# Performance work log

Hardware: AMD Instinct MI355X
Metric: run time of the kernel (lower is better)

The kernel has to match this reference:

```python
import jax, jax.numpy as jnp
import numpy as np

BZ, IN_DIM, STATE_DIM, OUT_DIM, L = 16, 512, 512, 512, 2048
INIT_SCALE = 0.5


def setup_inputs() -> dict:
    key = jax.random.key(0)
    k_u, k_a, k_b, k_c = jax.random.split(key, 4)
    u = jax.random.normal(k_u, (BZ, IN_DIM, L), dtype=jnp.float32)
    A_unconstrained = jax.random.normal(k_a, (STATE_DIM,), dtype=jnp.float32) * 0.1
    B = jax.random.normal(k_b, (STATE_DIM, IN_DIM), dtype=jnp.float32) * INIT_SCALE / np.sqrt(IN_DIM)
    C = jax.random.normal(k_c, (OUT_DIM, STATE_DIM), dtype=jnp.float32) * INIT_SCALE / np.sqrt(STATE_DIM)
    D = jnp.zeros((OUT_DIM, IN_DIM), dtype=jnp.float32)
    h0 = jnp.zeros((STATE_DIM,), dtype=jnp.float32)
    return {"u": u, "A_unconstrained": A_unconstrained, "B": B, "C": C, "D": D, "h0": h0}


def reference(u, A_unconstrained, B, C, D, h0):
    # u: (Bz, input_dim, L)
    Bz = u.shape[0]
    A_diag = -jax.nn.softplus(A_unconstrained)  # (S,)
    # Time-invariant input projection, batched over all timesteps: (L, Bz, S)
    Bu = jnp.einsum('bil,si->lbs', u, B)

    state0 = jnp.broadcast_to(h0[None, :], (Bz, h0.shape[0]))

    def step(state, bu_t):
        x_t = state * A_diag[None, :] + bu_t  # (Bz, S)
        return x_t, x_t

    _, xs = jax.lax.scan(step, state0, Bu)  # xs: (L, Bz, S)

    # Output projection: y_t = C x_t + D u_t  -> (Bz, out, L)
    Y = jnp.einsum('lbs,os->bol', xs, C) + jnp.einsum('bil,oi->bol', u, D)
    return Y
```

## Files before the change

### kernel.cpp

```cpp
#include <hip/hip_runtime.h>
#include <math.h>

typedef __bf16 bf16;
typedef __bf16 bf16x2 __attribute__((ext_vector_type(2)));
typedef __bf16 bf16x4 __attribute__((ext_vector_type(4)));
typedef __bf16 bf16x8 __attribute__((ext_vector_type(8)));
typedef float  f32x4  __attribute__((ext_vector_type(4)));

#define BZd 16
#define INd 512
#define Sd  512
#define Od  512
#define Ld  2048
#define CLd 128
#define NCd (Ld / CLd)

__global__ __launch_bounds__(256) void prep_all(const float* __restrict__ B,
                                                const float* __restrict__ C,
                                                const float* __restrict__ D,
                                                const float* __restrict__ Au,
                                                bf16* __restrict__ Bb, bf16* __restrict__ Cb,
                                                bf16* __restrict__ Db, float* __restrict__ A_diag,
                                                int* __restrict__ dfa) {
    __shared__ int sred[4];
    int bid = blockIdx.x;
    if (bid == 768) {
        #pragma unroll
        for (int r = 0; r < 2; ++r) {
            int ss = threadIdx.x + r * 256;
            float x = Au[ss];
            float sp = fmaxf(x, 0.0f) + log1pf(expf(-fabsf(x)));
            A_diag[ss] = -sp;
        }
        return;
    }
    int which = bid >> 8, lb = bid & 255;
    const float* src = which == 0 ? B : (which == 1 ? C : D);
    bf16* dst = which == 0 ? Bb : (which == 1 ? Cb : Db);
    int i = lb * 256 + threadIdx.x;
    float4 v = *(const float4*)&src[(size_t)i * 4];
    bf16x4 o = { (bf16)v.x, (bf16)v.y, (bf16)v.z, (bf16)v.w };
    *(bf16x4*)&dst[(size_t)i * 4] = o;
    if (which == 2) {
        int nz = (v.x != 0.f) | (v.y != 0.f) | (v.z != 0.f) | (v.w != 0.f);
        unsigned long long bl = __ballot(nz);
        int wv = threadIdx.x >> 6;
        if ((threadIdx.x & 63) == 0) sred[wv] = (bl != 0ull);
        __syncthreads();
        if (threadIdx.x == 0) dfa[lb] = sred[0] | sred[1] | sred[2] | sred[3];
    }
}

__global__ __launch_bounds__(256) void transp_u(const float* __restrict__ u,
                                                bf16* __restrict__ ut) {
    __shared__ bf16 t[64][73];
    int b = blockIdx.z, i0 = blockIdx.y * 64, l0 = blockIdx.x * 64;
    int tid = threadIdx.x, tx = tid & 15, ty = tid >> 4;
    const float* ub = u + ((size_t)b * INd + i0) * Ld + l0;
    #pragma unroll
    for (int r = 0; r < 4; ++r) {
        int il = r * 16 + ty;
        float4 v = *(const float4*)&ub[(size_t)il * Ld + tx * 4];
        t[il][tx * 4 + 0] = (bf16)v.x;
        t[il][tx * 4 + 1] = (bf16)v.y;
        t[il][tx * 4 + 2] = (bf16)v.z;
        t[il][tx * 4 + 3] = (bf16)v.w;
    }
    __syncthreads();
    bf16* uo = ut + ((size_t)b * Ld + l0) * INd + i0;
    #pragma unroll
    for (int it = 0; it < 2; ++it) {
        int q = it * 256 + tid;
        int lr = q >> 3;
        int ic = (q & 7) * 8;
        bf16x8 o;
        #pragma unroll
        for (int e = 0; e < 8; ++e) o[e] = t[ic + e][lr];
        *(bf16x8*)&uo[(size_t)lr * INd + ic] = o;
    }
}

template<bool OBF16>
__global__ __launch_bounds__(512, 2) void gemm8p(
    const bf16* __restrict__ A0, size_t aBS0,
    const bf16* __restrict__ B0, size_t bBS0,
    const bf16* __restrict__ A1, size_t aBS1,
    const bf16* __restrict__ B1, size_t bBS1,
    const int* __restrict__ dfa,
    const float* __restrict__ A_diag, float* __restrict__ cePtr,
    void* __restrict__ OutV, size_t oBS, int ldOut,
    int NX, int NY)
{
    __shared__ bf16 lds[4 * 16384];
    const int tid = threadIdx.x;
    const int lane = tid & 63, w = tid >> 6;

    int nwg = gridDim.x, bid = blockIdx.x;
    int cpx = nwg >> 3;
    int swz = (bid & 7) * cpx + (bid >> 3);
    int pb = NX * NY;
    int b  = swz / pb;
    int r0 = swz - b * pb;
    int by = r0 / NX;
    int bx = r0 - by * NX;

    const int wm = w >> 2, wn = w & 3;
    const int fr = lane & 15, g = lane >> 4;

    int extra = 0;
    if (dfa) {
        int4 f = ((const int4*)dfa)[lane];
        extra = __any((f.x | f.y | f.z | f.w) != 0) ? 1 : 0;
    }
    const int NT = extra ? 16 : 8;
    const int NU = 2 * NT;

    const bf16* Ab0 = A0 + (size_t)b * aBS0 + (size_t)(by * 256) * 512;
    const bf16* Bb0 = B0 + (size_t)b * bBS0 + (size_t)(bx * 256) * 512;
    const bf16* Ab1 = A1 + (size_t)b * aBS1 + (size_t)(by * 256) * 512;
    const bf16* Bb1 = B1 + (size_t)b * bBS1 + (size_t)(bx * 256) * 512;

    f32x4 acc[8][4];
    #pragma unroll
    for (int i = 0; i < 8; ++i)
        #pragma unroll
        for (int j = 0; j < 4; ++j)
            acc[i][j] = (f32x4){0.f, 0.f, 0.f, 0.f};

    auto stage_part = [&](int U, int isB) {
        int T = U >> 1, kh = U & 1;
        const bf16* Mb = isB ? (T >= 8 ? Bb1 : Bb0) : (T >= 8 ? Ab1 : Ab0);
        int kbase = ((T & 7) << 6) + (kh << 5);
        int slot = U & 3;
        #pragma unroll
        for (int rblk = 0; rblk < 2; ++rblk) {
            int row = rblk * 128 + (tid >> 2);
            int pos = tid & 3;
            int cs = pos ^ ((row & 3) ^ ((row >> 2) & 3));
            __builtin_amdgcn_global_load_lds(
                (const __attribute__((address_space(1))) void*)(Mb + (size_t)row * 512 + kbase + cs * 8),
                (__attribute__((address_space(3))) void*)&lds[slot * 16384 + isB * 8192 + (rblk * 128 + w * 16) * 32],
                16, 0, 0);
        }
    };

    stage_part(0, 0); stage_part(0, 1);
    stage_part(1, 0); stage_part(1, 1);
    stage_part(2, 0); stage_part(2, 1);

    bf16x8 av[4], bv[4];
    for (int U = 0; U < NU; ++U) {
        int ahead = NU - 1 - U;
        if (ahead >= 2)      { asm volatile("s_waitcnt vmcnt(8)" ::: "memory"); }
        else if (ahead == 1) { asm volatile("s_waitcnt vmcnt(4)" ::: "memory"); }
        else                 { asm volatile("s_waitcnt vmcnt(0)" ::: "memory"); }
        __builtin_amdgcn_sched_barrier(0);
        __builtin_amdgcn_s_barrier();
        __builtin_amdgcn_sched_barrier(0);

        const bf16* Ls = &lds[(U & 3) * 16384];
        #pragma unroll
        for (int mf = 0; mf < 2; ++mf) {
            if (mf == 1) {
                __builtin_amdgcn_sched_barrier(0);
                __builtin_amdgcn_s_barrier();
                __builtin_amdgcn_sched_barrier(0);
            }
            if (mf == 0) {
                #pragma unroll
                for (int j = 0; j < 4; ++j) {
                    int R = wn * 64 + j * 16 + fr;
                    int pos = g ^ ((R & 3) ^ ((R >> 2) & 3));
                    bv[j] = *(const bf16x8*)&Ls[8192 + R * 32 + pos * 8];
                }
            }
            #pragma unroll
            for (int i = 0; i < 4; ++i) {
                int R = wm * 128 + (mf * 4 + i) * 16 + fr;
                int pos = g ^ ((R & 3) ^ ((R >> 2) & 3));
                av[i] = *(const bf16x8*)&Ls[R * 32 + pos * 8];
            }
            if (U + 3 < NU) stage_part(U + 3, mf);
            asm volatile("s_waitcnt lgkmcnt(0)" ::: "memory");
            __builtin_amdgcn_sched_barrier(0);
            __builtin_amdgcn_s_setprio(1);
            #pragma unroll
            for (int i = 0; i < 4; ++i)
                #pragma unroll
                for (int j = 0; j < 4; ++j)
                    acc[mf * 4 + i][j] = __builtin_amdgcn_mfma_f32_16x16x32_bf16(
                        av[i], bv[j], acc[mf * 4 + i][j], 0, 0, 0);
            __builtin_amdgcn_s_setprio(0);
        }
    }

    if (OBF16 && cePtr) {
        int colBase = bx * 256 + wn * 64;
        #pragma unroll
        for (int j = 0; j < 4; ++j) {
            float a = A_diag[colBase + j * 16 + fr];
            float a2 = a * a, a4 = a2 * a2, a8 = a4 * a4, a16 = a8 * a8;
            float S = 0.f;
            #pragma unroll
            for (int I = 0; I < 8; ++I) {
                f32x4 v = acc[I][j];
                float e = fmaf(fmaf(fmaf(v[0], a, v[1]), a, v[2]), a, v[3]);
                float e0 = __shfl(e, fr);
                float e1 = __shfl(e, fr + 16);
                float e2 = __shfl(e, fr + 32);
                float e3 = __shfl(e, fr + 48);
                float E = fmaf(fmaf(fmaf(e0, a4, e1), a4, e2), a4, e3);
                S = fmaf(S, a16, E);
            }
            if (g == 0)
                cePtr[((size_t)b * NCd + (by * 2 + wm)) * Sd + colBase + j * 16 + fr] = S;
        }
    }

    int m0 = by * 256 + wm * 128 + g * 4;
    int n0 = bx * 256 + wn * 64 + fr;
    if (OBF16) {
        bf16* out = (bf16*)OutV + (size_t)b * oBS;
        #pragma unroll
        for (int i = 0; i < 8; ++i)
            #pragma unroll
            for (int j = 0; j < 4; ++j)
                #pragma unroll
                for (int q = 0; q < 4; ++q)
                    out[(size_t)(m0 + i * 16 + q) * ldOut + n0 + j * 16] = (bf16)acc[i][j][q];
    } else {
        float* out = (float*)OutV + (size_t)b * oBS;
        #pragma unroll
        for (int i = 0; i < 8; ++i)
            #pragma unroll
            for (int j = 0; j < 4; ++j)
                #pragma unroll
                for (int q = 0; q < 4; ++q)
                    out[(size_t)(m0 + i * 16 + q) * ldOut + n0 + j * 16] = acc[i][j][q];
    }
}

__global__ __launch_bounds__(256) void pass_scan2(bf16* __restrict__ xbuf,
                                                  const float* __restrict__ A_diag,
                                                  const float* __restrict__ ce,
                                                  const float* __restrict__ h0) {
    int gI = blockIdx.x * 256 + threadIdx.x;
    int sp = gI & 255;
    int c = (gI >> 8) & (NCd - 1);
    int b = gI >> 12;
    int s = sp * 2;
    float a0 = A_diag[s], a1 = A_diag[s + 1];
    float acl0 = a0, acl1 = a1;
    #pragma unroll
    for (int i = 0; i < 7; ++i) { acl0 *= acl0; acl1 *= acl1; }
    float x0 = h0[s], x1 = h0[s + 1];
    for (int cp = 0; cp < NCd; ++cp) {
        if (cp >= c) break;
        float2 e = *(const float2*)&ce[((size_t)b * NCd + cp) * Sd + s];
        x0 = fmaf(acl0, x0, e.x);
        x1 = fmaf(acl1, x1, e.y);
    }
    bf16* p = xbuf + ((size_t)b * Ld + (size_t)c * CLd) * Sd + s;
    #pragma unroll 4
    for (int j = 0; j < CLd; ++j) {
        bf16x2 v = *(const bf16x2*)&p[(size_t)j * Sd];
        x0 = fmaf(a0, x0, (float)v[0]);
        x1 = fmaf(a1, x1, (float)v[1]);
        bf16x2 o = { (bf16)x0, (bf16)x1 };
        *(bf16x2*)&p[(size_t)j * Sd] = o;
    }
}

extern "C" void kernel_launch(void* const* d_in, const int* in_sizes, int n_in,
                              void* d_out, int out_size, void* d_ws, size_t ws_size,
                              hipStream_t stream) {
    const float* u  = (const float*)d_in[0];
    const float* Au = (const float*)d_in[1];
    const float* Bm = (const float*)d_in[2];
    const float* Cm = (const float*)d_in[3];
    const float* Dm = (const float*)d_in[4];
    const float* h0 = (const float*)d_in[5];
    float* Y = (float*)d_out;

    char* ws = (char*)d_ws;
    bf16* bu = (bf16*)ws;
    bf16* ut = (bf16*)(ws + (32ull << 20));
    bf16* Bb = (bf16*)(ws + (64ull << 20));
    bf16* Cb = Bb + 262144;
    bf16* Db = Cb + 262144;
    float* A_diag = (float*)(ws + (64ull << 20) + 3ull * 524288);
    float* ce   = A_diag + 512;
    int*   dfa  = (int*)(ce + (size_t)BZd * NCd * Sd);

    prep_all<<<769, 256, 0, stream>>>(Bm, Cm, Dm, Au, Bb, Cb, Db, A_diag, dfa);
    transp_u<<<dim3(Ld / 64, INd / 64, BZd), 256, 0, stream>>>(u, ut);

    gemm8p<true><<<(Sd / 256) * (Ld / 256) * BZd, 512, 0, stream>>>(
        ut, (size_t)Ld * INd, Bb, 0,
        ut, (size_t)Ld * INd, Bb, 0,
        nullptr,
        A_diag, ce,
        (void*)bu, (size_t)Ld * Sd, Sd,
        Sd / 256, Ld / 256);

    pass_scan2<<<(BZd * NCd * (Sd / 2)) / 256, 256, 0, stream>>>(bu, A_diag, ce, h0);

    gemm8p<false><<<(Ld / 256) * (Od / 256) * BZd, 512, 0, stream>>>(
        Cb, 0, bu, (size_t)Ld * Sd,
        Db, 0, ut, (size_t)Ld * INd,
        dfa,
        A_diag, nullptr,
        (void*)Y, (size_t)Od * Ld, Ld,
        Ld / 256, Od / 256);
}
```

Before: 97.25 us.

## Fuse u transpose into GEMM and chunk scan into GEMM epilogue with decoupled lookback

Removes the separate transpose kernel by loading fp32 u directly in the first GEMM, transposing and converting it through registers into LDS. Removes the separate scan kernel by doing the intra-tile scan in the GEMM epilogue and chaining carries between tiles via global flags with spin-waits. The D-term is also handled in a separate fallback loop that reads u directly. This cuts two launches and a full read/write pass over the bf16 state buffer, but relies on co-residency of the tiles for the flag spin and adds serialization along the L dimension.

```diff
diff --git a/kernel.cpp b/kernel.cpp
--- a/kernel.cpp
+++ b/kernel.cpp
@@ -2,7 +2,6 @@
 #include <math.h>
 
 typedef __bf16 bf16;
-typedef __bf16 bf16x2 __attribute__((ext_vector_type(2)));
 typedef __bf16 bf16x4 __attribute__((ext_vector_type(4)));
 typedef __bf16 bf16x8 __attribute__((ext_vector_type(8)));
 typedef float  f32x4  __attribute__((ext_vector_type(4)));
@@ -12,8 +11,8 @@
 #define Sd  512
 #define Od  512
 #define Ld  2048
-#define CLd 128
-#define NCd (Ld / CLd)
+
+__device__ __forceinline__ int keyf(int r) { return (r & 3) ^ ((r >> 2) & 3); }
 
 __global__ __launch_bounds__(256) void prep_all(const float* __restrict__ B,
                                                 const float* __restrict__ C,
@@ -21,7 +20,7 @@
                                                 const float* __restrict__ Au,
                                                 bf16* __restrict__ Bb, bf16* __restrict__ Cb,
                                                 bf16* __restrict__ Db, float* __restrict__ A_diag,
-                                                int* __restrict__ dfa) {
+                                                int* __restrict__ dfa, int* __restrict__ flags) {
     __shared__ int sred[4];
     int bid = blockIdx.x;
     if (bid == 768) {
@@ -32,17 +31,18 @@
             float sp = fmaxf(x, 0.0f) + log1pf(expf(-fabsf(x)));
             A_diag[ss] = -sp;
         }
+        flags[threadIdx.x] = 0;
         return;
     }
     int which = bid >> 8, lb = bid & 255;
     const float* src = which == 0 ? B : (which == 1 ? C : D);
     bf16* dst = which == 0 ? Bb : (which == 1 ? Cb : Db);
     int i = lb * 256 + threadIdx.x;
-    float4 v = *(const float4*)&src[(size_t)i * 4];
-    bf16x4 o = { (bf16)v.x, (bf16)v.y, (bf16)v.z, (bf16)v.w };
+    f32x4 v = *(const f32x4*)&src[(size_t)i * 4];
+    bf16x4 o = { (bf16)v[0], (bf16)v[1], (bf16)v[2], (bf16)v[3] };
     *(bf16x4*)&dst[(size_t)i * 4] = o;
     if (which == 2) {
-        int nz = (v.x != 0.f) | (v.y != 0.f) | (v.z != 0.f) | (v.w != 0.f);
+        int nz = (v[0] != 0.f) | (v[1] != 0.f) | (v[2] != 0.f) | (v[3] != 0.f);
         unsigned long long bl = __ballot(nz);
         int wv = threadIdx.x >> 6;
         if ((threadIdx.x & 63) == 0) sred[wv] = (bl != 0ull);
@@ -51,47 +51,24 @@
     }
 }
 
-__global__ __launch_bounds__(256) void transp_u(const float* __restrict__ u,
-                                                bf16* __restrict__ ut) {
-    __shared__ bf16 t[64][73];
-    int b = blockIdx.z, i0 = blockIdx.y * 64, l0 = blockIdx.x * 64;
-    int tid = threadIdx.x, tx = tid & 15, ty = tid >> 4;
-    const float* ub = u + ((size_t)b * INd + i0) * Ld + l0;
-    #pragma unroll
-    for (int r = 0; r < 4; ++r) {
-        int il = r * 16 + ty;
-        float4 v = *(const float4*)&ub[(size_t)il * Ld + tx * 4];
-        t[il][tx * 4 + 0] = (bf16)v.x;
-        t[il][tx * 4 + 1] = (bf16)v.y;
-        t[il][tx * 4 + 2] = (bf16)v.z;
-        t[il][tx * 4 + 3] = (bf16)v.w;
-    }
-    __syncthreads();
-    bf16* uo = ut + ((size_t)b * Ld + l0) * INd + i0;
-    #pragma unroll
-    for (int it = 0; it < 2; ++it) {
-        int q = it * 256 + tid;
-        int lr = q >> 3;
-        int ic = (q & 7) * 8;
-        bf16x8 o;
-        #pragma unroll
-        for (int e = 0; e < 8; ++e) o[e] = t[ic + e][lr];
-        *(bf16x8*)&uo[(size_t)lr * INd + ic] = o;
-    }
-}
-
-template<bool OBF16>
+template<int AREG, int SCAN>
 __global__ __launch_bounds__(512, 2) void gemm8p(
-    const bf16* __restrict__ A0, size_t aBS0,
-    const bf16* __restrict__ B0, size_t bBS0,
-    const bf16* __restrict__ A1, size_t aBS1,
-    const bf16* __restrict__ B1, size_t bBS1,
+    const bf16* __restrict__ Abf, size_t aBS,
+    const float* __restrict__ Uf, size_t uBS,
+    const bf16* __restrict__ Bbf, size_t bBS,
+    const bf16* __restrict__ Dbf,
     const int* __restrict__ dfa,
-    const float* __restrict__ A_diag, float* __restrict__ cePtr,
+    const float* __restrict__ A_diag,
+    const float* __restrict__ h0,
+    float* __restrict__ Lg, int* __restrict__ flags,
     void* __restrict__ OutV, size_t oBS, int ldOut,
     int NX, int NY)
 {
-    __shared__ bf16 lds[4 * 16384];
+    constexpr int RS   = AREG ? 40 : 32;
+    constexpr int ASZ  = 256 * RS;
+    constexpr int SLOT = ASZ + 256 * 32;
+    __shared__ bf16 lds[4 * SLOT];
+
     const int tid = threadIdx.x;
     const int lane = tid & 63, w = tid >> 6;
 
@@ -106,19 +83,17 @@
 
     const int wm = w >> 2, wn = w & 3;
     const int fr = lane & 15, g = lane >> 4;
+    const int iq = tid & 7, lq = tid >> 3;
+
+    const bf16*  Ab = AREG ? nullptr : (Abf + (size_t)b * aBS + (size_t)(by * 256) * 512);
+    const float* Ub = Uf ? (Uf + (size_t)b * uBS) : nullptr;
+    const bf16*  Bp = Bbf + (size_t)b * bBS + (size_t)(bx * 256) * 512;
 
     int extra = 0;
-    if (dfa) {
+    if (!AREG && dfa) {
         int4 f = ((const int4*)dfa)[lane];
         extra = __any((f.x | f.y | f.z | f.w) != 0) ? 1 : 0;
     }
-    const int NT = extra ? 16 : 8;
-    const int NU = 2 * NT;
-
-    const bf16* Ab0 = A0 + (size_t)b * aBS0 + (size_t)(by * 256) * 512;
-    const bf16* Bb0 = B0 + (size_t)b * bBS0 + (size_t)(bx * 256) * 512;
-    const bf16* Ab1 = A1 + (size_t)b * aBS1 + (size_t)(by * 256) * 512;
-    const bf16* Bb1 = B1 + (size_t)b * bBS1 + (size_t)(bx * 256) * 512;
 
     f32x4 acc[8][4];
     #pragma unroll
@@ -127,99 +102,225 @@
         for (int j = 0; j < 4; ++j)
             acc[i][j] = (f32x4){0.f, 0.f, 0.f, 0.f};
 
-    auto stage_part = [&](int U, int isB) {
-        int T = U >> 1, kh = U & 1;
-        const bf16* Mb = isB ? (T >= 8 ? Bb1 : Bb0) : (T >= 8 ? Ab1 : Ab0);
-        int kbase = ((T & 7) << 6) + (kh << 5);
-        int slot = U & 3;
-        #pragma unroll
-        for (int rblk = 0; rblk < 2; ++rblk) {
-            int row = rblk * 128 + (tid >> 2);
-            int pos = tid & 3;
-            int cs = pos ^ ((row & 3) ^ ((row >> 2) & 3));
-            __builtin_amdgcn_global_load_lds(
-                (const __attribute__((address_space(1))) void*)(Mb + (size_t)row * 512 + kbase + cs * 8),
-                (__attribute__((address_space(3))) void*)&lds[slot * 16384 + isB * 8192 + (rblk * 128 + w * 16) * 32],
-                16, 0, 0);
-        }
-    };
-
-    stage_part(0, 0); stage_part(0, 1);
-    stage_part(1, 0); stage_part(1, 1);
-    stage_part(2, 0); stage_part(2, 1);
-
-    bf16x8 av[4], bv[4];
-    for (int U = 0; U < NU; ++U) {
-        int ahead = NU - 1 - U;
-        if (ahead >= 2)      { asm volatile("s_waitcnt vmcnt(8)" ::: "memory"); }
-        else if (ahead == 1) { asm volatile("s_waitcnt vmcnt(4)" ::: "memory"); }
-        else                 { asm volatile("s_waitcnt vmcnt(0)" ::: "memory"); }
+    f32x4 areg[4];
+
+    #define GLD16(srcP, dstElem) __builtin_amdgcn_global_load_lds( \
+        (const __attribute__((address_space(1))) void*)(srcP), \
+        (__attribute__((address_space(3))) void*)&lds[dstElem], 16, 0, 0)
+
+    auto gldA = [&](int U) {
+        #pragma unroll
+        for (int rb = 0; rb < 2; ++rb) {
+            int row = rb * 128 + (tid >> 2);
+            int cs = (tid & 3) ^ keyf(row);
+            GLD16(Ab + (size_t)row * 512 + U * 32 + cs * 8,
+                  (U & 3) * SLOT + (rb * 128 + w * 16) * 32);
+        }
+    };
+    auto gldB = [&](int U) {
+        #pragma unroll
+        for (int rb = 0; rb < 2; ++rb) {
+            int row = rb * 128 + (tid >> 2);
+            int cs = (tid & 3) ^ keyf(row);
+            GLD16(Bp + (size_t)row * 512 + U * 32 + cs * 8,
+                  (U & 3) * SLOT + ASZ + (rb * 128 + w * 16) * 32);
+        }
+    };
+    auto issueA = [&](int U) {
+        #pragma unroll
+        for (int d = 0; d < 4; ++d)
+            areg[d] = *(const f32x4*)&Ub[(size_t)(U * 32 + iq * 4 + d) * Ld + by * 256 + lq * 4];
+    };
+    auto writeA = [&](int U) {
+        bf16* As = &lds[(U & 3) * SLOT];
+        #pragma unroll
+        for (int dl = 0; dl < 4; ++dl) {
+            int r = lq * 4 + dl;
+            bf16x4 wv = { (bf16)areg[0][dl], (bf16)areg[1][dl], (bf16)areg[2][dl], (bf16)areg[3][dl] };
+            *(bf16x4*)&As[r * RS + iq * 4] = wv;
+        }
+    };
+    auto readFrags = [&](int slot, bf16x8* avf, bf16x8* bvf) {
+        const bf16* As = &lds[slot * SLOT];
+        const bf16* Bs = &lds[slot * SLOT + ASZ];
+        #pragma unroll
+        for (int i = 0; i < 8; ++i) {
+            int R = wm * 128 + i * 16 + fr;
+            if (AREG) avf[i] = *(const bf16x8*)&As[R * RS + g * 8];
+            else      avf[i] = *(const bf16x8*)&As[R * RS + (g ^ keyf(R)) * 8];
+        }
+        #pragma unroll
+        for (int j = 0; j < 4; ++j) {
+            int R = wn * 64 + j * 16 + fr;
+            bvf[j] = *(const bf16x8*)&Bs[R * 32 + (g ^ keyf(R)) * 8];
+        }
+    };
+
+    if (AREG) { issueA(0); gldB(0); gldB(1); }
+    else      { gldA(0); gldB(0); gldA(1); gldB(1); }
+
+    for (int U = 0; U < 16; ++U) {
+        if (U < 15) {
+            if (AREG) asm volatile("s_waitcnt vmcnt(2)" ::: "memory");
+            else      asm volatile("s_waitcnt vmcnt(4)" ::: "memory");
+        } else {
+            asm volatile("s_waitcnt vmcnt(0)" ::: "memory");
+        }
         __builtin_amdgcn_sched_barrier(0);
+        if (AREG) {
+            writeA(U);
+            asm volatile("s_waitcnt lgkmcnt(0)" ::: "memory");
+        }
         __builtin_amdgcn_s_barrier();
         __builtin_amdgcn_sched_barrier(0);
-
-        const bf16* Ls = &lds[(U & 3) * 16384];
-        #pragma unroll
-        for (int mf = 0; mf < 2; ++mf) {
-            if (mf == 1) {
-                __builtin_amdgcn_sched_barrier(0);
+        bf16x8 av[8], bv[4];
+        readFrags(U & 3, av, bv);
+        if (AREG) { if (U + 1 < 16) issueA(U + 1); }
+        else      { if (U + 2 < 16) gldA(U + 2); }
+        if (U + 2 < 16) gldB(U + 2);
+        __builtin_amdgcn_s_setprio(1);
+        #pragma unroll
+        for (int i = 0; i < 8; ++i)
+            #pragma unroll
+            for (int j = 0; j < 4; ++j)
+                acc[i][j] = __builtin_amdgcn_mfma_f32_16x16x32_bf16(av[i], bv[j], acc[i][j], 0, 0, 0);
+        __builtin_amdgcn_s_setprio(0);
+    }
+
+    if (!AREG) {
+        if (extra) {
+            #pragma unroll 1
+            for (int T = 0; T < 16; ++T) {
+                int k0 = T * 32;
                 __builtin_amdgcn_s_barrier();
-                __builtin_amdgcn_sched_barrier(0);
+                f32x4 r4[4];
+                #pragma unroll
+                for (int d = 0; d < 4; ++d)
+                    r4[d] = *(const f32x4*)&Ub[(size_t)(k0 + iq * 4 + d) * Ld + bx * 256 + lq * 4];
+                #pragma unroll
+                for (int rb = 0; rb < 2; ++rb) {
+                    int row = rb * 128 + (tid >> 2);
+                    int cs = (tid & 3) ^ keyf(row);
+                    GLD16(Dbf + (size_t)(by * 256 + row) * 512 + k0 + cs * 8,
+                          (rb * 128 + w * 16) * 32);
+                }
+                asm volatile("s_waitcnt vmcnt(0)" ::: "memory");
+                #pragma unroll
+                for (int dl = 0; dl < 4; ++dl) {
+                    int r = lq * 4 + dl;
+                    bf16x4 wv = { (bf16)r4[0][dl], (bf16)r4[1][dl], (bf16)r4[2][dl], (bf16)r4[3][dl] };
+                    int e = ((iq >> 1) ^ keyf(r)) * 8 + (iq & 1) * 4;
+                    *(bf16x4*)&lds[ASZ + r * 32 + e] = wv;
+                }
+                asm volatile("s_waitcnt lgkmcnt(0)" ::: "memory");
+                __builtin_amdgcn_s_barrier();
+                bf16x8 av[8], bv[4];
+                readFrags(0, av, bv);
+                #pragma unroll
+                for (int i = 0; i < 8; ++i)
+                    #pragma unroll
+                    for (int j = 0; j < 4; ++j)
+                        acc[i][j] = __builtin_amdgcn_mfma_f32_16x16x32_bf16(av[i], bv[j], acc[i][j], 0, 0, 0);
             }
-            if (mf == 0) {
-                #pragma unroll
-                for (int j = 0; j < 4; ++j) {
-                    int R = wn * 64 + j * 16 + fr;
-                    int pos = g ^ ((R & 3) ^ ((R >> 2) & 3));
-                    bv[j] = *(const bf16x8*)&Ls[8192 + R * 32 + pos * 8];
-                }
+        }
+    }
+
+    int n0 = bx * 256 + wn * 64 + fr;
+    int m0 = by * 256 + wm * 128 + g * 4;
+
+    if (SCAN) {
+        float av_[4], a2_[4], a4_[4], a16_[4], a128_[4], a256_[4], A4G_[4];
+        #pragma unroll
+        for (int j = 0; j < 4; ++j) {
+            float a = A_diag[n0 + j * 16];
+            float a2 = a * a, a4 = a2 * a2, a8 = a4 * a4, a16 = a8 * a8;
+            float a32 = a16 * a16, a64 = a32 * a32, a128 = a64 * a64;
+            av_[j] = a; a2_[j] = a2; a4_[j] = a4; a16_[j] = a16;
+            a128_[j] = a128; a256_[j] = a128 * a128;
+            A4G_[j] = (g == 0) ? 1.0f : (g == 1) ? a4 : (g == 2) ? a8 : a8 * a4;
+        }
+        float P8[4];
+        #pragma unroll
+        for (int j = 0; j < 4; ++j) {
+            float a = av_[j], a4 = a4_[j], a16 = a16_[j];
+            float P = 0.0f;
+            #pragma unroll
+            for (int i = 0; i < 8; ++i) {
+                f32x4 v = acc[i][j];
+                float e = fmaf(fmaf(fmaf(v[0], a, v[1]), a, v[2]), a, v[3]);
+                float e0 = __shfl(e, fr), e1 = __shfl(e, fr + 16);
+                float e2 = __shfl(e, fr + 32), e3 = __shfl(e, fr + 48);
+                float E = fmaf(fmaf(fmaf(e0, a4, e1), a4, e2), a4, e3);
+                float h2 = fmaf(e0, a4, e1), h3 = fmaf(h2, a4, e2);
+                float PG = (g == 0) ? 0.0f : (g == 1) ? e0 : (g == 2) ? h2 : h3;
+                float Vg = fmaf(A4G_[j], P, PG);
+                float x0 = fmaf(a, Vg, v[0]);
+                float x1 = fmaf(a, x0, v[1]);
+                float x2 = fmaf(a, x1, v[2]);
+                float x3 = fmaf(a, x2, v[3]);
+                acc[i][j] = (f32x4){x0, x1, x2, x3};
+                P = fmaf(P, a16, E);
             }
-            #pragma unroll
-            for (int i = 0; i < 4; ++i) {
-                int R = wm * 128 + (mf * 4 + i) * 16 + fr;
-                int pos = g ^ ((R & 3) ^ ((R >> 2) & 3));
-                av[i] = *(const bf16x8*)&Ls[R * 32 + pos * 8];
+            P8[j] = P;
+        }
+        float* sc = (float*)lds;
+        __syncthreads();
+        if (wm == 0 && g == 0) {
+            #pragma unroll
+            for (int j = 0; j < 4; ++j) sc[wn * 64 + j * 16 + fr] = P8[j];
+        }
+        __syncthreads();
+        float L0[4] = {0.f, 0.f, 0.f, 0.f};
+        if (wm == 1) {
+            #pragma unroll
+            for (int j = 0; j < 4; ++j) L0[j] = sc[wn * 64 + j * 16 + fr];
+        }
+        int fbase = (b * NX + bx) * 8;
+        size_t lbase = ((size_t)(fbase + by)) * 256;
+        if (wm == 1 && g == 0) {
+            #pragma unroll
+            for (int j = 0; j < 4; ++j)
+                __hip_atomic_store(&Lg[lbase + wn * 64 + j * 16 + fr],
+                                   fmaf(L0[j], a128_[j], P8[j]),
+                                   __ATOMIC_RELAXED, __HIP_MEMORY_SCOPE_AGENT);
+        }
+        __syncthreads();
+        __threadfence();
+        if (tid == 0)
+            __hip_atomic_store(&flags[fbase + by], 1, __ATOMIC_RELEASE, __HIP_MEMORY_SCOPE_AGENT);
+        float W[4];
+        #pragma unroll
+        for (int j = 0; j < 4; ++j) W[j] = h0[n0 + j * 16];
+        for (int k = 0; k < by; ++k) {
+            while (__hip_atomic_load(&flags[fbase + k], __ATOMIC_ACQUIRE, __HIP_MEMORY_SCOPE_AGENT) == 0)
+                __builtin_amdgcn_s_sleep(2);
+            size_t lk = ((size_t)(fbase + k)) * 256;
+            #pragma unroll
+            for (int j = 0; j < 4; ++j) {
+                float Lk = __hip_atomic_load(&Lg[lk + wn * 64 + j * 16 + fr],
+                                             __ATOMIC_RELAXED, __HIP_MEMORY_SCOPE_AGENT);
+                W[j] = fmaf(W[j], a256_[j], Lk);
             }
-            if (U + 3 < NU) stage_part(U + 3, mf);
-            asm volatile("s_waitcnt lgkmcnt(0)" ::: "memory");
-            __builtin_amdgcn_sched_barrier(0);
-            __builtin_amdgcn_s_setprio(1);
-            #pragma unroll
-            for (int i = 0; i < 4; ++i)
-                #pragma unroll
-                for (int j = 0; j < 4; ++j)
-                    acc[mf * 4 + i][j] = __builtin_amdgcn_mfma_f32_16x16x32_bf16(
-                        av[i], bv[j], acc[mf * 4 + i][j], 0, 0, 0);
-            __builtin_amdgcn_s_setprio(0);
-        }
-    }
-
-    if (OBF16 && cePtr) {
-        int colBase = bx * 256 + wn * 64;
+        }
         #pragma unroll
         for (int j = 0; j < 4; ++j) {
-            float a = A_diag[colBase + j * 16 + fr];
-            float a2 = a * a, a4 = a2 * a2, a8 = a4 * a4, a16 = a8 * a8;
-            float S = 0.f;
-            #pragma unroll
-            for (int I = 0; I < 8; ++I) {
-                f32x4 v = acc[I][j];
-                float e = fmaf(fmaf(fmaf(v[0], a, v[1]), a, v[2]), a, v[3]);
-                float e0 = __shfl(e, fr);
-                float e1 = __shfl(e, fr + 16);
-                float e2 = __shfl(e, fr + 32);
-                float e3 = __shfl(e, fr + 48);
-                float E = fmaf(fmaf(fmaf(e0, a4, e1), a4, e2), a4, e3);
-                S = fmaf(S, a16, E);
+            float Wh = (wm == 0) ? W[j] : fmaf(W[j], a128_[j], L0[j]);
+            float a = av_[j], a2 = a2_[j], a3 = a2 * a, a4 = a4_[j];
+            float pw = A4G_[j] * Wh;
+            #pragma unroll
+            for (int i = 0; i < 8; ++i) {
+                f32x4 x = acc[i][j];
+                x[0] = fmaf(pw, a,  x[0]);
+                x[1] = fmaf(pw, a2, x[1]);
+                x[2] = fmaf(pw, a3, x[2]);
+                x[3] = fmaf(pw, a4, x[3]);
+                acc[i][j] = x;
+                pw *= a16_[j];
             }
-            if (g == 0)
-                cePtr[((size_t)b * NCd + (by * 2 + wm)) * Sd + colBase + j * 16 + fr] = S;
-        }
-    }
-
-    int m0 = by * 256 + wm * 128 + g * 4;
-    int n0 = bx * 256 + wn * 64 + fr;
-    if (OBF16) {
+        }
+    }
+
+    if (SCAN) {
         bf16* out = (bf16*)OutV + (size_t)b * oBS;
         #pragma unroll
         for (int i = 0; i < 8; ++i)
@@ -238,37 +339,7 @@
                 for (int q = 0; q < 4; ++q)
                     out[(size_t)(m0 + i * 16 + q) * ldOut + n0 + j * 16] = acc[i][j][q];
     }
-}
-
-__global__ __launch_bounds__(256) void pass_scan2(bf16* __restrict__ xbuf,
-                                                  const float* __restrict__ A_diag,
-                                                  const float* __restrict__ ce,
-                                                  const float* __restrict__ h0) {
-    int gI = blockIdx.x * 256 + threadIdx.x;
-    int sp = gI & 255;
-    int c = (gI >> 8) & (NCd - 1);
-    int b = gI >> 12;
-    int s = sp * 2;
-    float a0 = A_diag[s], a1 = A_diag[s + 1];
-    float acl0 = a0, acl1 = a1;
-    #pragma unroll
-    for (int i = 0; i < 7; ++i) { acl0 *= acl0; acl1 *= acl1; }
-    float x0 = h0[s], x1 = h0[s + 1];
-    for (int cp = 0; cp < NCd; ++cp) {
-        if (cp >= c) break;
-        float2 e = *(const float2*)&ce[((size_t)b * NCd + cp) * Sd + s];
-        x0 = fmaf(acl0, x0, e.x);
-        x1 = fmaf(acl1, x1, e.y);
-    }
-    bf16* p = xbuf + ((size_t)b * Ld + (size_t)c * CLd) * Sd + s;
-    #pragma unroll 4
-    for (int j = 0; j < CLd; ++j) {
-        bf16x2 v = *(const bf16x2*)&p[(size_t)j * Sd];
-        x0 = fmaf(a0, x0, (float)v[0]);
-        x1 = fmaf(a1, x1, (float)v[1]);
-        bf16x2 o = { (bf16)x0, (bf16)x1 };
-        *(bf16x2*)&p[(size_t)j * Sd] = o;
-    }
+    #undef GLD16
 }
 
 extern "C" void kernel_launch(void* const* d_in, const int* in_sizes, int n_in,
@@ -283,33 +354,26 @@
     float* Y = (float*)d_out;
 
     char* ws = (char*)d_ws;
-    bf16* bu = (bf16*)ws;
-    bf16* ut = (bf16*)(ws + (32ull << 20));
-    bf16* Bb = (bf16*)(ws + (64ull << 20));
+    bf16* xs = (bf16*)ws;
+    bf16* Bb = (bf16*)(ws + (32ull << 20));
     bf16* Cb = Bb + 262144;
     bf16* Db = Cb + 262144;
-    float* A_diag = (float*)(ws + (64ull << 20) + 3ull * 524288);
-    float* ce   = A_diag + 512;
-    int*   dfa  = (int*)(ce + (size_t)BZd * NCd * Sd);
-
-    prep_all<<<769, 256, 0, stream>>>(Bm, Cm, Dm, Au, Bb, Cb, Db, A_diag, dfa);
-    transp_u<<<dim3(Ld / 64, INd / 64, BZd), 256, 0, stream>>>(u, ut);
-
-    gemm8p<true><<<(Sd / 256) * (Ld / 256) * BZd, 512, 0, stream>>>(
-        ut, (size_t)Ld * INd, Bb, 0,
-        ut, (size_t)Ld * INd, Bb, 0,
-        nullptr,
-        A_diag, ce,
-        (void*)bu, (size_t)Ld * Sd, Sd,
+    float* A_diag = (float*)(ws + (32ull << 20) + 3ull * 524288);
+    float* Lg     = A_diag + 512;
+    int*   flags  = (int*)(Lg + 16 * 2 * 8 * 256);
+    int*   dfa    = flags + 256;
+
+    prep_all<<<769, 256, 0, stream>>>(Bm, Cm, Dm, Au, Bb, Cb, Db, A_diag, dfa, flags);
+
+    gemm8p<1, 1><<<(Sd / 256) * (Ld / 256) * BZd, 512, 0, stream>>>(
+        nullptr, 0, u, (size_t)INd * Ld, Bb, 0, nullptr,
+        nullptr, A_diag, h0, Lg, flags,
+        (void*)xs, (size_t)Ld * Sd, Sd,
         Sd / 256, Ld / 256);
 
-    pass_scan2<<<(BZd * NCd * (Sd / 2)) / 256, 256, 0, stream>>>(bu, A_diag, ce, h0);
-
-    gemm8p<false><<<(Ld / 256) * (Od / 256) * BZd, 512, 0, stream>>>(
-        Cb, 0, bu, (size_t)Ld * Sd,
-        Db, 0, ut, (size_t)Ld * INd,
-        dfa,
-        A_diag, nullptr,
+    gemm8p<0, 0><<<(Ld / 256) * (Od / 256) * BZd, 512, 0, stream>>>(
+        Cb, 0, u, (size_t)INd * Ld, xs, (size_t)Ld * Sd, Db,
+        dfa, A_diag, h0, nullptr, nullptr,
         (void*)Y, (size_t)Od * Ld, Ld,
         Ld / 256, Od / 256);
 }
```

Result: slower. 160.9 us (median of 3 runs) (+65.5%).
